# Optimization experiments

Hardware: AMD Instinct MI355X
Metric: run time of the kernel (lower is better)

The kernel has to match this reference:

```python
import jax, jax.numpy as jnp
import numpy as np


def setup_inputs() -> dict:
    key = jax.random.key(0)
    k1, k2, k3, k4 = jax.random.split(key, 4)
    B, S, D, F = 16, 4096, 1024, 1024
    x = jax.random.normal(k1, (B, S, D), dtype=jnp.float32)
    # Keras 'normal' initializer ~ N(0, 0.05); scale similarly for realism
    W_key = jax.random.normal(k2, (D, F), dtype=jnp.float32) * 0.05
    W_query = jax.random.normal(k3, (D, F), dtype=jnp.float32) * 0.05
    W_value = jax.random.normal(k4, (D, F), dtype=jnp.float32) * 0.05
    return {"x": x, "W_key": W_key, "W_query": W_query, "W_value": W_value}


def reference(x, W_key, W_query, W_value):
    # x: [B,S,D]; W_*: [D,F]
    keys = jnp.tanh(jnp.einsum("bsd,df->bsf", x, W_key))
    query = jnp.tanh(jnp.einsum("bsd,df->bsf", x, W_query))
    value = jnp.tanh(jnp.einsum("bsd,df->bsf", x, W_value))
    # diag(Q K^T) == per-token dot product, computed directly in O(S*F)
    attn_scores = jnp.einsum("bsf,bsf->bs", query, keys)  # [B,S]
    attn_softmax = jax.nn.softmax(attn_scores, axis=-1)[..., None]  # [B,S,1]
    # value^T @ softmax -> [B,F,1]
    weighted_input = jnp.einsum("bsf,bso->bfo", value, attn_softmax)
    return weighted_input, attn_softmax
```

## Files before the change

### kernel.cpp

```cpp
#include <hip/hip_runtime.h>
#include <hip/hip_bf16.h>
#include <math.h>
#include <stdint.h>

typedef _Float16 f16;
typedef _Float16 half8 __attribute__((ext_vector_type(8)));
typedef float f32x4 __attribute__((ext_vector_type(4)));

#define B_ 16
#define S_ 4096
#define D_ 1024
#define F_ 1024
#define TOK (B_*S_)
#define TB3 128
#define FB3 64
#define NFB3 16
#define NT3 32
#define NSV 4
#define CSV (S_/NSV)

__device__ __forceinline__ void gload_lds16(const void* g, void* l) {
    __builtin_amdgcn_global_load_lds(
        (__attribute__((address_space(1))) const unsigned int*)(unsigned long long)(uintptr_t)g,
        (__attribute__((address_space(3))) unsigned int*)(unsigned int)(uintptr_t)l,
        16, 0, 0);
}

__device__ __forceinline__ void fma2(float2& a, float s, const float2& wv) {
    a.x += s * wv.x; a.y += s * wv.y;
}

__global__ void cvt_x(const float* __restrict__ x, f16* __restrict__ xh) {
    size_t i = ((size_t)blockIdx.x * 256 + threadIdx.x) * 8;
    float4 a = *(const float4*)(x + i);
    float4 b = *(const float4*)(x + i + 4);
    half8 h = {(f16)a.x,(f16)a.y,(f16)a.z,(f16)a.w,
               (f16)b.x,(f16)b.y,(f16)b.z,(f16)b.w};
    *(half8*)(xh + i) = h;
}

__global__ void cvt_w2(const float* __restrict__ Wk, const float* __restrict__ Wq,
                       f16* __restrict__ wtf) {
    const int gw   = blockIdx.x * 4 + (threadIdx.x >> 6);
    const int lane = threadIdx.x & 63;
    const int nblk = gw & 3, kt = (gw >> 2) & 31, fb = (gw >> 7) & 15, mat = gw >> 11;
    const float* W = mat ? Wq : Wk;
    const int f  = fb * 64 + nblk * 16 + (lane & 15);
    const int d0 = kt * 32 + (lane >> 4) * 8;
    half8 h;
#pragma unroll
    for (int e = 0; e < 8; ++e) h[e] = (f16)W[(size_t)(d0 + e) * F_ + f];
    *(half8*)(wtf + (size_t)gw * 512 + lane * 8) = h;
}

__launch_bounds__(256, 4)
__global__ void score_gemm(const f16* __restrict__ xh, const f16* __restrict__ wtf,
                           float* __restrict__ part) {
    __shared__ __align__(16) f16 Xs[4][TB3 * 32];
    __shared__ float sred[2][TB3];

    const int hid  = blockIdx.x;
    const int orig = (hid & 7) * 1024 + (hid >> 3);
    const int fb   = orig & 15;
    const int tok0 = (orig >> 4) * TB3;

    const int t = threadIdx.x, lane = t & 63, w = t >> 6;
    const int wr = (w >> 1) * 64;
    const int wc = (w & 1) * 32;

    const int rx0 = t >> 2,         qx0 = (t & 3) ^ ((rx0 >> 1) & 3);
    const int rx1 = (t + 256) >> 2, qx1 = (t & 3) ^ ((rx1 >> 1) & 3);
    const f16* srcX0 = xh + (size_t)(tok0 + rx0) * D_ + qx0 * 8;
    const f16* srcX1 = xh + (size_t)(tok0 + rx1) * D_ + qx1 * 8;
    const int wbase = w * 1024;

    int offA[4];
#pragma unroll
    for (int m = 0; m < 4; ++m) {
        int row = wr + m * 16 + (lane & 15);
        int q   = (lane >> 4) ^ ((row >> 1) & 3);
        offA[m] = row * 32 + q * 8;
    }

    const f16* bK = wtf + (((size_t)fb * NT3 * 4) + 2 * (w & 1)) * 512 + lane * 8;
    const f16* bQ = bK + (size_t)NFB3 * NT3 * 4 * 512;

#define STAGE_X(sl, kof) do {                                         \
        gload_lds16(srcX0 + (kof), (char*)Xs[sl] + wbase);            \
        gload_lds16(srcX1 + (kof), (char*)Xs[sl] + 4096 + wbase);     \
    } while (0)

    f32x4 accK[4][2] = {};
    f32x4 accQ[4][2] = {};
    half8 wKf[2][2], wQf[2][2];

    STAGE_X(0, 0);
    STAGE_X(1, 32);
    STAGE_X(2, 64);
#pragma unroll
    for (int n = 0; n < 2; ++n) {
        wKf[0][n] = *(const half8*)(bK + n * 512);
        wQf[0][n] = *(const half8*)(bQ + n * 512);
    }
    asm volatile("s_waitcnt vmcnt(8)" ::: "memory");
    __builtin_amdgcn_s_barrier();

#pragma unroll
    for (int kt = 0; kt < NT3; ++kt) {
        const int cur = kt & 3, par = kt & 1, nx = par ^ 1;
        if (kt < NT3 - 1) {
#pragma unroll
            for (int n = 0; n < 2; ++n) {
                wKf[nx][n] = *(const half8*)(bK + ((size_t)(kt + 1) * 4 + n) * 512);
                wQf[nx][n] = *(const half8*)(bQ + ((size_t)(kt + 1) * 4 + n) * 512);
            }
        }
        if (kt < NT3 - 3) STAGE_X((kt + 3) & 3, (kt + 3) * 32);

        half8 aF[4];
#pragma unroll
        for (int m = 0; m < 4; ++m) aF[m] = *(const half8*)(Xs[cur] + offA[m]);
#pragma unroll
        for (int n = 0; n < 2; ++n)
#pragma unroll
            for (int m = 0; m < 4; ++m) {
                accK[m][n] = __builtin_amdgcn_mfma_f32_16x16x32_f16(aF[m], wKf[par][n], accK[m][n], 0, 0, 0);
                accQ[m][n] = __builtin_amdgcn_mfma_f32_16x16x32_f16(aF[m], wQf[par][n], accQ[m][n], 0, 0, 0);
            }
        if (kt < NT3 - 1) __builtin_amdgcn_s_barrier();
    }
#undef STAGE_X

#pragma unroll
    for (int m = 0; m < 4; ++m) {
        float s[4] = {0.f, 0.f, 0.f, 0.f};
#pragma unroll
        for (int n = 0; n < 2; ++n)
#pragma unroll
            for (int j = 0; j < 4; ++j)
                s[j] += tanhf(accQ[m][n][j]) * tanhf(accK[m][n][j]);
#pragma unroll
        for (int j = 0; j < 4; ++j) {
            s[j] += __shfl_xor(s[j], 1);
            s[j] += __shfl_xor(s[j], 2);
            s[j] += __shfl_xor(s[j], 4);
            s[j] += __shfl_xor(s[j], 8);
        }
        if ((lane & 15) == 0) {
            int g = lane >> 4;
#pragma unroll
            for (int j = 0; j < 4; ++j)
                sred[w & 1][wr + m * 16 + g * 4 + j] = s[j];
        }
    }
    __syncthreads();
    if (t < TB3)
        part[(size_t)fb * TOK + tok0 + t] = sred[0][t] + sred[1][t];
}

__global__ void sum_k(const float* __restrict__ part, float* __restrict__ scores) {
    int i = blockIdx.x * 256 + threadIdx.x;
    float s = 0.f;
#pragma unroll
    for (int fb = 0; fb < NFB3; ++fb) s += part[(size_t)fb * TOK + i];
    scores[i] = s;
}

__global__ void softmax_k(const float* __restrict__ scores, float* __restrict__ out) {
    __shared__ float sc[S_];
    __shared__ float red[256];
    const int b = blockIdx.x, t = threadIdx.x;
    float lmax = -1e30f;
    for (int i = t; i < S_; i += 256) {
        float s = scores[(size_t)b * S_ + i];
        sc[i] = s;
        lmax = fmaxf(lmax, s);
    }
    red[t] = lmax; __syncthreads();
    for (int o = 128; o > 0; o >>= 1) { if (t < o) red[t] = fmaxf(red[t], red[t + o]); __syncthreads(); }
    const float mx = red[0]; __syncthreads();
    float lsum = 0.f;
    for (int i = t; i < S_; i += 256) { float e = expf(sc[i] - mx); sc[i] = e; lsum += e; }
    red[t] = lsum; __syncthreads();
    for (int o = 128; o > 0; o >>= 1) { if (t < o) red[t] += red[t + o]; __syncthreads(); }
    const float inv = 1.0f / red[0];
    for (int i = t; i < S_; i += 256)
        out[(size_t)B_ * F_ + (size_t)b * S_ + i] = sc[i] * inv;
}

__launch_bounds__(512)
__global__ void value_k5(const float* __restrict__ x, const float* __restrict__ Wv,
                         const float* __restrict__ p_in, float* __restrict__ vpart) {
    __shared__ __align__(16) float xs[8][D_];
    __shared__ float ps[CSV];
    __shared__ int   idxs[CSV];
    __shared__ int   wsum[8];
    __shared__ int   rbase_s;
    const int b = blockIdx.x, c = blockIdx.y;
    const int t = threadIdx.x, lane = t & 63, w = t >> 6;
    const int s0 = c * CSV;

    if (t == 0) rbase_s = 0;
    __syncthreads();
#pragma unroll 1
    for (int r = 0; r < 2; ++r) {
        int i = r * 512 + t;
        float p = p_in[(size_t)b * S_ + s0 + i];
        bool flag = p > 1e-7f;
        unsigned long long mask = __ballot(flag);
        if (lane == 0) wsum[w] = __popcll(mask);
        __syncthreads();
        int base = rbase_s;
#pragma unroll
        for (int k = 0; k < 8; ++k) if (k < w) base += wsum[k];
        if (flag) {
            int pos = base + __popcll(mask & ((1ull << lane) - 1ull));
            idxs[pos] = s0 + i;
            ps[pos] = p;
        }
        __syncthreads();
        if (t == 0) {
            int sum = 0;
#pragma unroll
            for (int k = 0; k < 8; ++k) sum += wsum[k];
            rbase_s += sum;
        }
        __syncthreads();
    }
    const int cnt = rbase_s;

    float2 acc = {0.f, 0.f};
    for (int g = 0; g < cnt; g += 8) {
        __syncthreads();
        const int ng = cnt - g;
#pragma unroll
        for (int r = 0; r < 8; ++r) {
            float2 v = {0.f, 0.f};
            if (r < ng)
                v = ((const float2*)(x + ((size_t)b * S_ + idxs[g + r]) * D_))[t];
            ((float2*)xs[r])[t] = v;
        }
        __syncthreads();
        if (ng >= 5) {
            float2 a[8] = {};
#pragma unroll 2
            for (int dq = 0; dq < D_ / 4; ++dq) {
                const float* wrp = Wv + (size_t)dq * 4 * F_ + 2 * t;
                float2 wv0 = *(const float2*)(wrp         );
                float2 wv1 = *(const float2*)(wrp + F_    );
                float2 wv2 = *(const float2*)(wrp + 2 * F_);
                float2 wv3 = *(const float2*)(wrp + 3 * F_);
#pragma unroll
                for (int r = 0; r < 8; ++r) {
                    float4 xr = ((const float4*)xs[r])[dq];
                    fma2(a[r], xr.x, wv0); fma2(a[r], xr.y, wv1);
                    fma2(a[r], xr.z, wv2); fma2(a[r], xr.w, wv3);
                }
            }
#pragma unroll
            for (int r = 0; r < 8; ++r)
                if (g + r < cnt) {
                    float pw = ps[g + r];
                    acc.x += pw * tanhf(a[r].x);
                    acc.y += pw * tanhf(a[r].y);
                }
        } else {
            float2 a[4] = {};
#pragma unroll 2
            for (int dq = 0; dq < D_ / 4; ++dq) {
                const float* wrp = Wv + (size_t)dq * 4 * F_ + 2 * t;
                float2 wv0 = *(const float2*)(wrp         );
                float2 wv1 = *(const float2*)(wrp + F_    );
                float2 wv2 = *(const float2*)(wrp + 2 * F_);
                float2 wv3 = *(const float2*)(wrp + 3 * F_);
#pragma unroll
                for (int r = 0; r < 4; ++r) {
                    float4 xr = ((const float4*)xs[r])[dq];
                    fma2(a[r], xr.x, wv0); fma2(a[r], xr.y, wv1);
                    fma2(a[r], xr.z, wv2); fma2(a[r], xr.w, wv3);
                }
            }
#pragma unroll
            for (int r = 0; r < 4; ++r)
                if (g + r < cnt) {
                    float pw = ps[g + r];
                    acc.x += pw * tanhf(a[r].x);
                    acc.y += pw * tanhf(a[r].y);
                }
        }
    }
    ((float2*)(vpart + ((size_t)c * B_ + b) * F_))[t] = acc;
}

__global__ void value_red(const float* __restrict__ vpart, float* __restrict__ out) {
    int i = blockIdx.x * 256 + threadIdx.x;
    float s = 0.f;
#pragma unroll
    for (int c = 0; c < NSV; ++c) s += vpart[(size_t)c * B_ * F_ + i];
    out[i] = s;
}

extern "C" void kernel_launch(void* const* d_in, const int* in_sizes, int n_in,
                              void* d_out, int out_size, void* d_ws, size_t ws_size,
                              hipStream_t stream) {
    const float* x  = (const float*)d_in[0];
    const float* Wk = (const float*)d_in[1];
    const float* Wq = (const float*)d_in[2];
    const float* Wv = (const float*)d_in[3];
    float* out = (float*)d_out;
    char* ws = (char*)d_ws;

    f16*   xh     = (f16*)ws;
    f16*   wtf    = (f16*)(ws + (size_t)TOK * D_ * 2);
    float* part   = (float*)(ws + (size_t)TOK * D_ * 2 + 2 * (size_t)D_ * F_ * 2);
    float* scores = part + (size_t)NFB3 * TOK;

    cvt_x<<<TOK * D_ / 8 / 256, 256, 0, stream>>>(x, xh);
    cvt_w2<<<1024, 256, 0, stream>>>(Wk, Wq, wtf);
    score_gemm<<<NFB3 * (TOK / TB3), 256, 0, stream>>>(xh, wtf, part);
    sum_k<<<TOK / 256, 256, 0, stream>>>(part, scores);
    softmax_k<<<B_, 256, 0, stream>>>(scores, out);
    float* vpart = part;
    const float* p_in = out + (size_t)B_ * F_;
    value_k5<<<dim3(B_, NSV), 512, 0, stream>>>(x, Wv, p_in, vpart);
    value_red<<<B_ * F_ / 256, 256, 0, stream>>>(vpart, out);
}
```

Measured before the change: 553.3 us.

## Enlarge score GEMM tile to 256x128 with 8 waves and 4-phase pipelined k-loop

Grows the score GEMM block tile from 128 tokens x 64 features to 256 tokens x 128 features with 512 threads, using a K-step of 64 staged in a 4-deep LDS ring with an XOR swizzle. The weight fragments are re-laid out per wave-column slice, and each K-step is split into four phases with barriers and s_setprio around the MFMA bursts. Per-wave partial scores go straight to global memory, so the cross-wave LDS reduction is gone but the number of partial slices doubles to 32. The goal is more reuse of X and W per byte loaded and fewer blocks in total. The cost is lower occupancy, more barriers per step, and twice as many partials for sum_k to read.

```diff
diff --git a/kernel.cpp b/kernel.cpp
--- a/kernel.cpp
+++ b/kernel.cpp
@@ -12,10 +12,11 @@
 #define D_ 1024
 #define F_ 1024
 #define TOK (B_*S_)
-#define TB3 128
-#define FB3 64
-#define NFB3 16
-#define NT3 32
+#define TB5 256
+#define FB5 128
+#define NFB5 8
+#define NK5 16
+#define NSL 32
 #define NSV 4
 #define CSV (S_/NSV)
 
@@ -43,96 +44,106 @@
                        f16* __restrict__ wtf) {
     const int gw   = blockIdx.x * 4 + (threadIdx.x >> 6);
     const int lane = threadIdx.x & 63;
-    const int nblk = gw & 3, kt = (gw >> 2) & 31, fb = (gw >> 7) & 15, mat = gw >> 11;
+    const int nf = gw & 1, mat = (gw >> 1) & 1, kt32 = (gw >> 2) & 31, slice = gw >> 7;
+    const int fb = slice >> 2, wc = slice & 3;
     const float* W = mat ? Wq : Wk;
-    const int f  = fb * 64 + nblk * 16 + (lane & 15);
-    const int d0 = kt * 32 + (lane >> 4) * 8;
+    const int f  = fb * 128 + wc * 32 + nf * 16 + (lane & 15);
+    const int d0 = kt32 * 32 + (lane >> 4) * 8;
     half8 h;
 #pragma unroll
     for (int e = 0; e < 8; ++e) h[e] = (f16)W[(size_t)(d0 + e) * F_ + f];
     *(half8*)(wtf + (size_t)gw * 512 + lane * 8) = h;
 }
 
-__launch_bounds__(256, 4)
+__launch_bounds__(512, 2)
 __global__ void score_gemm(const f16* __restrict__ xh, const f16* __restrict__ wtf,
                            float* __restrict__ part) {
-    __shared__ __align__(16) f16 Xs[4][TB3 * 32];
-    __shared__ float sred[2][TB3];
+    __shared__ __align__(16) f16 Xs[4][TB5 * 64];
 
     const int hid  = blockIdx.x;
-    const int orig = (hid & 7) * 1024 + (hid >> 3);
-    const int fb   = orig & 15;
-    const int tok0 = (orig >> 4) * TB3;
+    const int orig = (hid & 7) * 256 + (hid >> 3);
+    const int fb   = orig & 7;
+    const int tok0 = (orig >> 3) * TB5;
 
     const int t = threadIdx.x, lane = t & 63, w = t >> 6;
-    const int wr = (w >> 1) * 64;
-    const int wc = (w & 1) * 32;
-
-    const int rx0 = t >> 2,         qx0 = (t & 3) ^ ((rx0 >> 1) & 3);
-    const int rx1 = (t + 256) >> 2, qx1 = (t & 3) ^ ((rx1 >> 1) & 3);
-    const f16* srcX0 = xh + (size_t)(tok0 + rx0) * D_ + qx0 * 8;
-    const f16* srcX1 = xh + (size_t)(tok0 + rx1) * D_ + qx1 * 8;
-    const int wbase = w * 1024;
-
-    int offA[4];
-#pragma unroll
-    for (int m = 0; m < 4; ++m) {
-        int row = wr + m * 16 + (lane & 15);
-        int q   = (lane >> 4) ^ ((row >> 1) & 3);
-        offA[m] = row * 32 + q * 8;
-    }
-
-    const f16* bK = wtf + (((size_t)fb * NT3 * 4) + 2 * (w & 1)) * 512 + lane * 8;
-    const f16* bQ = bK + (size_t)NFB3 * NT3 * 4 * 512;
-
-#define STAGE_X(sl, kof) do {                                         \
-        gload_lds16(srcX0 + (kof), (char*)Xs[sl] + wbase);            \
-        gload_lds16(srcX1 + (kof), (char*)Xs[sl] + 4096 + wbase);     \
-    } while (0)
-
-    f32x4 accK[4][2] = {};
-    f32x4 accQ[4][2] = {};
-    half8 wKf[2][2], wQf[2][2];
-
-    STAGE_X(0, 0);
-    STAGE_X(1, 32);
-    STAGE_X(2, 64);
-#pragma unroll
-    for (int n = 0; n < 2; ++n) {
-        wKf[0][n] = *(const half8*)(bK + n * 512);
-        wQf[0][n] = *(const half8*)(bQ + n * 512);
-    }
-    asm volatile("s_waitcnt vmcnt(8)" ::: "memory");
+    const int wr = (w >> 2) * 128;
+    const int wc = w & 3;
+
+    const int srow = t >> 3;
+    const int qsrc = (t & 7) ^ (srow & 7);
+    const f16* srcX[4];
+#pragma unroll
+    for (int i = 0; i < 4; ++i)
+        srcX[i] = xh + (size_t)(tok0 + i * 64 + srow) * D_ + qsrc * 8;
+
+    int rowb[8];
+#pragma unroll
+    for (int m = 0; m < 8; ++m)
+        rowb[m] = (wr + m * 16 + (lane & 15)) * 128;
+    const int kq0 = (((lane >> 4)    ) ^ (lane & 7)) * 16;
+    const int kq1 = (((lane >> 4) | 4) ^ (lane & 7)) * 16;
+
+    const f16* bW = wtf + (size_t)(fb * 4 + wc) * 128 * 512 + lane * 8;
+
+#define STAGE1(sl, kt, i_)                                                      \
+    gload_lds16(srcX[i_] + (size_t)(kt) * 64,                                   \
+                (char*)Xs[sl] + (i_) * 8192 + w * 1024)
+
+    f32x4 accK[8][2] = {};
+    f32x4 accQ[8][2] = {};
+    half8 wf[2][8];
+
+#pragma unroll
+    for (int i = 0; i < 4; ++i) STAGE1(0, 0, i);
+#pragma unroll
+    for (int i = 0; i < 4; ++i) STAGE1(1, 1, i);
+#pragma unroll
+    for (int i = 0; i < 4; ++i) STAGE1(2, 2, i);
+#pragma unroll
+    for (int j = 0; j < 8; ++j)
+        wf[0][j] = *(const half8*)(bW + (size_t)((j >> 2) * 4 + (j & 3)) * 512);
+    asm volatile("s_waitcnt vmcnt(16)" ::: "memory");
     __builtin_amdgcn_s_barrier();
 
 #pragma unroll
-    for (int kt = 0; kt < NT3; ++kt) {
+    for (int kt = 0; kt < NK5; ++kt) {
         const int cur = kt & 3, par = kt & 1, nx = par ^ 1;
-        if (kt < NT3 - 1) {
-#pragma unroll
-            for (int n = 0; n < 2; ++n) {
-                wKf[nx][n] = *(const half8*)(bK + ((size_t)(kt + 1) * 4 + n) * 512);
-                wQf[nx][n] = *(const half8*)(bQ + ((size_t)(kt + 1) * 4 + n) * 512);
+        const char* Xb = (const char*)Xs[cur];
+#pragma unroll
+        for (int p = 0; p < 4; ++p) {
+            const int ks = p >> 1, mh = p & 1;
+            if (kt < NK5 - 1) {
+                wf[nx][2*p]   = *(const half8*)(bW + ((size_t)(2*(kt+1) + (p >> 1)) * 4 + ((2*p)   & 3)) * 512);
+                wf[nx][2*p+1] = *(const half8*)(bW + ((size_t)(2*(kt+1) + (p >> 1)) * 4 + ((2*p+1) & 3)) * 512);
             }
-        }
-        if (kt < NT3 - 3) STAGE_X((kt + 3) & 3, (kt + 3) * 32);
-
-        half8 aF[4];
-#pragma unroll
-        for (int m = 0; m < 4; ++m) aF[m] = *(const half8*)(Xs[cur] + offA[m]);
-#pragma unroll
-        for (int n = 0; n < 2; ++n)
-#pragma unroll
-            for (int m = 0; m < 4; ++m) {
-                accK[m][n] = __builtin_amdgcn_mfma_f32_16x16x32_f16(aF[m], wKf[par][n], accK[m][n], 0, 0, 0);
-                accQ[m][n] = __builtin_amdgcn_mfma_f32_16x16x32_f16(aF[m], wQf[par][n], accQ[m][n], 0, 0, 0);
-            }
-        if (kt < NT3 - 1) __builtin_amdgcn_s_barrier();
-    }
-#undef STAGE_X
-
-#pragma unroll
-    for (int m = 0; m < 4; ++m) {
+            if (kt < NK5 - 3) STAGE1((kt + 3) & 3, kt + 3, p);
+
+            half8 aF[4];
+            const int kq = ks ? kq1 : kq0;
+#pragma unroll
+            for (int i = 0; i < 4; ++i)
+                aF[i] = *(const half8*)(Xb + rowb[mh * 4 + i] + kq);
+
+            __builtin_amdgcn_s_barrier();
+            asm volatile("s_waitcnt lgkmcnt(0)" ::: "memory");
+            __builtin_amdgcn_sched_barrier(0);
+            __builtin_amdgcn_s_setprio(1);
+#pragma unroll
+            for (int i = 0; i < 4; ++i)
+#pragma unroll
+                for (int n = 0; n < 2; ++n) {
+                    accK[mh*4+i][n] = __builtin_amdgcn_mfma_f32_16x16x32_f16(aF[i], wf[par][ks*4 + n],     accK[mh*4+i][n], 0, 0, 0);
+                    accQ[mh*4+i][n] = __builtin_amdgcn_mfma_f32_16x16x32_f16(aF[i], wf[par][ks*4 + 2 + n], accQ[mh*4+i][n], 0, 0, 0);
+                }
+            __builtin_amdgcn_s_setprio(0);
+            __builtin_amdgcn_s_barrier();
+        }
+    }
+#undef STAGE1
+
+    const int slice = fb * 4 + wc;
+#pragma unroll
+    for (int m = 0; m < 8; ++m) {
         float s[4] = {0.f, 0.f, 0.f, 0.f};
 #pragma unroll
         for (int n = 0; n < 2; ++n)
@@ -150,19 +161,16 @@
             int g = lane >> 4;
 #pragma unroll
             for (int j = 0; j < 4; ++j)
-                sred[w & 1][wr + m * 16 + g * 4 + j] = s[j];
-        }
-    }
-    __syncthreads();
-    if (t < TB3)
-        part[(size_t)fb * TOK + tok0 + t] = sred[0][t] + sred[1][t];
+                part[(size_t)slice * TOK + tok0 + wr + m * 16 + g * 4 + j] = s[j];
+        }
+    }
 }
 
 __global__ void sum_k(const float* __restrict__ part, float* __restrict__ scores) {
     int i = blockIdx.x * 256 + threadIdx.x;
     float s = 0.f;
 #pragma unroll
-    for (int fb = 0; fb < NFB3; ++fb) s += part[(size_t)fb * TOK + i];
+    for (int sl = 0; sl < NSL; ++sl) s += part[(size_t)sl * TOK + i];
     scores[i] = s;
 }
 
@@ -313,11 +321,11 @@
     f16*   xh     = (f16*)ws;
     f16*   wtf    = (f16*)(ws + (size_t)TOK * D_ * 2);
     float* part   = (float*)(ws + (size_t)TOK * D_ * 2 + 2 * (size_t)D_ * F_ * 2);
-    float* scores = part + (size_t)NFB3 * TOK;
+    float* scores = part + (size_t)NSL * TOK;
 
     cvt_x<<<TOK * D_ / 8 / 256, 256, 0, stream>>>(x, xh);
     cvt_w2<<<1024, 256, 0, stream>>>(Wk, Wq, wtf);
-    score_gemm<<<NFB3 * (TOK / TB3), 256, 0, stream>>>(xh, wtf, part);
+    score_gemm<<<NFB5 * (TOK / TB5), 512, 0, stream>>>(xh, wtf, part);
     sum_k<<<TOK / 256, 256, 0, stream>>>(part, scores);
     softmax_k<<<B_, 256, 0, stream>>>(scores, out);
     float* vpart = part;
```

Result: slower. 596.5 us (+7.8%).

## Fuse fp32-to-fp16 conversion of x into score GEMM staging

Applied to the files above, without the earlier changes.

Removes the separate cvt_x pass and its fp16 workspace copy. The score GEMM now loads fp32 x via registers, converts to fp16 and writes to swizzled LDS, with a two-buffer register prefetch pipeline. This avoids a full read/write pass over x but doubles the bytes the GEMM fetches per tile, replaces async global-to-LDS loads with register staging, and lowers occupancy to 3 blocks per CU.

```diff
diff --git a/kernel.cpp b/kernel.cpp
--- a/kernel.cpp
+++ b/kernel.cpp
@@ -19,24 +19,8 @@
 #define NSV 4
 #define CSV (S_/NSV)
 
-__device__ __forceinline__ void gload_lds16(const void* g, void* l) {
-    __builtin_amdgcn_global_load_lds(
-        (__attribute__((address_space(1))) const unsigned int*)(unsigned long long)(uintptr_t)g,
-        (__attribute__((address_space(3))) unsigned int*)(unsigned int)(uintptr_t)l,
-        16, 0, 0);
-}
-
 __device__ __forceinline__ void fma2(float2& a, float s, const float2& wv) {
     a.x += s * wv.x; a.y += s * wv.y;
-}
-
-__global__ void cvt_x(const float* __restrict__ x, f16* __restrict__ xh) {
-    size_t i = ((size_t)blockIdx.x * 256 + threadIdx.x) * 8;
-    float4 a = *(const float4*)(x + i);
-    float4 b = *(const float4*)(x + i + 4);
-    half8 h = {(f16)a.x,(f16)a.y,(f16)a.z,(f16)a.w,
-               (f16)b.x,(f16)b.y,(f16)b.z,(f16)b.w};
-    *(half8*)(xh + i) = h;
 }
 
 __global__ void cvt_w2(const float* __restrict__ Wk, const float* __restrict__ Wq,
@@ -53,8 +37,8 @@
     *(half8*)(wtf + (size_t)gw * 512 + lane * 8) = h;
 }
 
-__launch_bounds__(256, 4)
-__global__ void score_gemm(const f16* __restrict__ xh, const f16* __restrict__ wtf,
+__launch_bounds__(256, 3)
+__global__ void score_gemm(const float* __restrict__ x, const f16* __restrict__ wtf,
                            float* __restrict__ part) {
     __shared__ __align__(16) f16 Xs[4][TB3 * 32];
     __shared__ float sred[2][TB3];
@@ -68,11 +52,12 @@
     const int wr = (w >> 1) * 64;
     const int wc = (w & 1) * 32;
 
-    const int rx0 = t >> 2,         qx0 = (t & 3) ^ ((rx0 >> 1) & 3);
-    const int rx1 = (t + 256) >> 2, qx1 = (t & 3) ^ ((rx1 >> 1) & 3);
-    const f16* srcX0 = xh + (size_t)(tok0 + rx0) * D_ + qx0 * 8;
-    const f16* srcX1 = xh + (size_t)(tok0 + rx1) * D_ + qx1 * 8;
-    const int wbase = w * 1024;
+    const int r = t >> 1, h = t & 1;
+    const float* gx = x + (size_t)(tok0 + r) * D_ + h * 16;
+    const int qs0 = (h * 2)     ^ ((r >> 1) & 3);
+    const int qs1 = (h * 2 + 1) ^ ((r >> 1) & 3);
+    const int wb0 = r * 64 + qs0 * 16;
+    const int wb1 = r * 64 + qs1 * 16;
 
     int offA[4];
 #pragma unroll
@@ -85,29 +70,49 @@
     const f16* bK = wtf + (((size_t)fb * NT3 * 4) + 2 * (w & 1)) * 512 + lane * 8;
     const f16* bQ = bK + (size_t)NFB3 * NT3 * 4 * 512;
 
-#define STAGE_X(sl, kof) do {                                         \
-        gload_lds16(srcX0 + (kof), (char*)Xs[sl] + wbase);            \
-        gload_lds16(srcX1 + (kof), (char*)Xs[sl] + 4096 + wbase);     \
+#define LOADX(buf, kt) do {                                           \
+        const float4* s_ = (const float4*)(gx + (size_t)(kt) * 32);   \
+        buf[0] = s_[0]; buf[1] = s_[1]; buf[2] = s_[2]; buf[3] = s_[3];\
+    } while (0)
+#define WRITEX(sl, buf) do {                                                        \
+        half8 lo_ = {(f16)buf[0].x,(f16)buf[0].y,(f16)buf[0].z,(f16)buf[0].w,       \
+                     (f16)buf[1].x,(f16)buf[1].y,(f16)buf[1].z,(f16)buf[1].w};      \
+        half8 hi_ = {(f16)buf[2].x,(f16)buf[2].y,(f16)buf[2].z,(f16)buf[2].w,       \
+                     (f16)buf[3].x,(f16)buf[3].y,(f16)buf[3].z,(f16)buf[3].w};      \
+        *(half8*)((char*)Xs[sl] + wb0) = lo_;                                       \
+        *(half8*)((char*)Xs[sl] + wb1) = hi_;                                       \
     } while (0)
 
     f32x4 accK[4][2] = {};
     f32x4 accQ[4][2] = {};
     half8 wKf[2][2], wQf[2][2];
-
-    STAGE_X(0, 0);
-    STAGE_X(1, 32);
-    STAGE_X(2, 64);
+    float4 xrA[4], xrB[4];
+
+    LOADX(xrA, 0);
+    LOADX(xrB, 1);
 #pragma unroll
     for (int n = 0; n < 2; ++n) {
         wKf[0][n] = *(const half8*)(bK + n * 512);
         wQf[0][n] = *(const half8*)(bQ + n * 512);
     }
-    asm volatile("s_waitcnt vmcnt(8)" ::: "memory");
-    __builtin_amdgcn_s_barrier();
+    WRITEX(0, xrA);
+    LOADX(xrA, 2);
+    WRITEX(1, xrB);
+    LOADX(xrB, 3);
+    __syncthreads();
 
 #pragma unroll
     for (int kt = 0; kt < NT3; ++kt) {
         const int cur = kt & 3, par = kt & 1, nx = par ^ 1;
+
+        if (kt < NT3 - 2) {
+            if ((kt & 1) == 0) WRITEX((kt + 2) & 3, xrA);
+            else               WRITEX((kt + 2) & 3, xrB);
+        }
+        if (kt < NT3 - 4) {
+            if ((kt & 1) == 0) LOADX(xrA, kt + 4);
+            else               LOADX(xrB, kt + 4);
+        }
         if (kt < NT3 - 1) {
 #pragma unroll
             for (int n = 0; n < 2; ++n) {
@@ -115,7 +120,6 @@
                 wQf[nx][n] = *(const half8*)(bQ + ((size_t)(kt + 1) * 4 + n) * 512);
             }
         }
-        if (kt < NT3 - 3) STAGE_X((kt + 3) & 3, (kt + 3) * 32);
 
         half8 aF[4];
 #pragma unroll
@@ -129,7 +133,8 @@
             }
         if (kt < NT3 - 1) __builtin_amdgcn_s_barrier();
     }
-#undef STAGE_X
+#undef LOADX
+#undef WRITEX
 
 #pragma unroll
     for (int m = 0; m < 4; ++m) {
@@ -310,14 +315,12 @@
     float* out = (float*)d_out;
     char* ws = (char*)d_ws;
 
-    f16*   xh     = (f16*)ws;
-    f16*   wtf    = (f16*)(ws + (size_t)TOK * D_ * 2);
-    float* part   = (float*)(ws + (size_t)TOK * D_ * 2 + 2 * (size_t)D_ * F_ * 2);
+    f16*   wtf    = (f16*)ws;
+    float* part   = (float*)(ws + 2 * (size_t)D_ * F_ * 2);
     float* scores = part + (size_t)NFB3 * TOK;
 
-    cvt_x<<<TOK * D_ / 8 / 256, 256, 0, stream>>>(x, xh);
     cvt_w2<<<1024, 256, 0, stream>>>(Wk, Wq, wtf);
-    score_gemm<<<NFB3 * (TOK / TB3), 256, 0, stream>>>(xh, wtf, part);
+    score_gemm<<<NFB3 * (TOK / TB3), 256, 0, stream>>>(x, wtf, part);
     sum_k<<<TOK / 256, 256, 0, stream>>>(part, scores);
     softmax_k<<<B_, 256, 0, stream>>>(scores, out);
     float* vpart = part;
```

Result: slower. 587.7 us (+6.2%).
